# Kernel optimization log

Hardware: AMD Instinct MI355X
Metric: run time of the kernel (lower is better)

Reference implementation:

```python
import jax, jax.numpy as jnp
import numpy as np

B, A, D = 256, 128, 5          # batch, max_atoms, max_degree
FA, FB, C = 256, 64, 256       # atom feats, bond feats, conv_width


def setup_inputs() -> dict:
    key = jax.random.key(0)
    k1, k2, k3, k4 = jax.random.split(key, 4)
    atoms = jax.random.normal(k1, (B, A, FA), dtype=jnp.float32)
    bonds = jax.random.normal(k2, (B, A, D, FB), dtype=jnp.float32)
    # neighbour indices with -1 as padding value
    edges = jax.random.randint(k3, (B, A, D), -1, A, dtype=jnp.int32)
    W = jax.random.normal(k4, (D, FA + FB, C), dtype=jnp.float32) * 0.05
    b = jnp.zeros((D, C), dtype=jnp.float32)
    return {"atoms": atoms, "bonds": bonds, "edges": edges, "W": W, "b": b}


def reference(atoms, bonds, edges, W, b):
    # atom degree = number of non-padding neighbours  (B, A)
    deg = jnp.sum(edges != -1, axis=-1)

    # neighbour_lookup: pad a zero atom at index 0, shift indices by +1 so -1 -> 0
    masked_atoms = jnp.pad(atoms, ((0, 0), (1, 0), (0, 0)))        # (B, A+1, FA)
    idx = edges + 1                                                # (B, A, D)
    neigh = masked_atoms[jnp.arange(B)[:, None, None], idx]        # (B, A, D, FA)

    # include_self=True then sum over neighbour axis == self + sum(neighbours)
    summed_atom = atoms + jnp.sum(neigh, axis=2)                   # (B, A, FA)
    summed_bond = jnp.sum(bonds, axis=2)                           # (B, A, FB)
    feat = jnp.concatenate([summed_atom, summed_bond], axis=-1)    # (B, A, FA+FB)

    # per-degree Dense (relu), masked by (degree == d), summed over degrees
    dense = jax.nn.relu(jnp.einsum('baf,dfc->badc', feat, W) + b)  # (B, A, D, C)
    mask = (deg[..., None] == jnp.arange(D)).astype(dense.dtype)   # (B, A, D)
    return jnp.einsum('badc,bad->bac', dense, mask)                # (B, A, C)
```

## Files before the change

kernel.cpp:

```cpp
#include <hip/hip_runtime.h>


#define NB 256
#define NA 128
#define ND 5
#define NFA 256
#define NFB 64
#define NC 256
#define NF (NFA + NFB)

__global__ __launch_bounds__(256) void ngh_kernel(
    const float* __restrict__ atoms,
    const float* __restrict__ bonds,
    const int*   __restrict__ edges,
    const float* __restrict__ W,
    const float* __restrict__ bias,
    float* __restrict__ out)
{
    const int row = blockIdx.x;
    const int b   = row >> 7;
    const int a   = row & (NA - 1);
    const int t   = threadIdx.x;

    int e[ND];
    int deg = 0;
#pragma unroll
    for (int d = 0; d < ND; ++d) {
        e[d] = edges[row * ND + d];
        deg += (e[d] != -1) ? 1 : 0;
    }

    float* orow = out + (size_t)row * NC;

    if (deg >= ND) {
        orow[t] = 0.0f;
        return;
    }

    __shared__ float feat[NF];
    {
        const float* arow = atoms + ((size_t)b * NA + a) * NFA;
        float v = arow[t];
#pragma unroll
        for (int d = 0; d < ND; ++d) {
            if (e[d] != -1) {
                v += atoms[((size_t)b * NA + e[d]) * NFA + t];
            }
        }
        feat[t] = v;
    }
    if (t < NFB) {
        const float* brow = bonds + ((size_t)b * NA + a) * (ND * NFB);
        float v = 0.0f;
#pragma unroll
        for (int d = 0; d < ND; ++d) v += brow[d * NFB + t];
        feat[NFA + t] = v;
    }
    __syncthreads();

    const float* Wd = W + (size_t)deg * NF * NC + t;
    float acc = bias[deg * NC + t];
#pragma unroll 8
    for (int f = 0; f < NF; ++f) {
        acc = fmaf(feat[f], Wd[(size_t)f * NC], acc);
    }
    orow[t] = fmaxf(acc, 0.0f);
}

extern "C" void kernel_launch(void* const* d_in, const int* in_sizes, int n_in,
                              void* d_out, int out_size, void* d_ws, size_t ws_size,
                              hipStream_t stream) {
    const float* atoms = (const float*)d_in[0];
    const float* bonds = (const float*)d_in[1];
    const int*   edges = (const int*)  d_in[2];
    const float* W     = (const float*)d_in[3];
    const float* bias  = (const float*)d_in[4];
    float*       out   = (float*)d_out;

    dim3 grid(NB * NA);
    dim3 block(NC);
    ngh_kernel<<<grid, block, 0, stream>>>(atoms, bonds, edges, W, bias, out);
}
```

Baseline: 134.3 us.

## Bucket rows by degree and batch four rows per block for shared W reuse

A scan kernel zeroes the output and sorts row indices into per-degree lists with atomics. A persistent gather-matmul kernel then processes four same-degree rows per block, so each W element loaded is reused across four rows instead of one. This cuts W traffic roughly fourfold, at the cost of an extra memset, an extra launch and atomic list building. It falls back to the old kernel when no workspace is available.

New measurement: 147.9 us. 10.1% more time.

```diff
diff --git a/kernel.cpp b/kernel.cpp
--- a/kernel.cpp
+++ b/kernel.cpp
@@ -8,14 +8,14 @@
 #define NFB 64
 #define NC 256
 #define NF (NFA + NFB)
+#define NROWS (NB * NA)
+#define RPB 16
+#define RPC 4
 
 __global__ __launch_bounds__(256) void ngh_kernel(
-    const float* __restrict__ atoms,
-    const float* __restrict__ bonds,
-    const int*   __restrict__ edges,
-    const float* __restrict__ W,
-    const float* __restrict__ bias,
-    float* __restrict__ out)
+    const float* __restrict__ atoms, const float* __restrict__ bonds,
+    const int* __restrict__ edges, const float* __restrict__ W,
+    const float* __restrict__ bias, float* __restrict__ out)
 {
     const int row = blockIdx.x;
     const int b   = row >> 7;
@@ -31,22 +31,15 @@
     }
 
     float* orow = out + (size_t)row * NC;
-
-    if (deg >= ND) {
-        orow[t] = 0.0f;
-        return;
-    }
+    if (deg >= ND) { orow[t] = 0.0f; return; }
 
     __shared__ float feat[NF];
     {
         const float* arow = atoms + ((size_t)b * NA + a) * NFA;
         float v = arow[t];
 #pragma unroll
-        for (int d = 0; d < ND; ++d) {
-            if (e[d] != -1) {
-                v += atoms[((size_t)b * NA + e[d]) * NFA + t];
-            }
-        }
+        for (int d = 0; d < ND; ++d)
+            if (e[d] != -1) v += atoms[((size_t)b * NA + e[d]) * NFA + t];
         feat[t] = v;
     }
     if (t < NFB) {
@@ -61,10 +54,111 @@
     const float* Wd = W + (size_t)deg * NF * NC + t;
     float acc = bias[deg * NC + t];
 #pragma unroll 8
-    for (int f = 0; f < NF; ++f) {
-        acc = fmaf(feat[f], Wd[(size_t)f * NC], acc);
+    for (int f = 0; f < NF; ++f) acc = fmaf(feat[f], Wd[(size_t)f * NC], acc);
+    orow[t] = fmaxf(acc, 0.0f);
+}
+
+__global__ __launch_bounds__(256) void scan_zero_kernel(
+    const int* __restrict__ edges, float* __restrict__ out,
+    int* __restrict__ cnt, int* __restrict__ list)
+{
+    const int t  = threadIdx.x;
+    const int r0 = blockIdx.x * RPB;
+
+    float4* dst = reinterpret_cast<float4*>(out + (size_t)r0 * NC);
+    const float4 z = make_float4(0.f, 0.f, 0.f, 0.f);
+#pragma unroll
+    for (int k = 0; k < (RPB * NC / 4) / 256; ++k) dst[t + k * 256] = z;
+
+    if (t < RPB) {
+        const int row = r0 + t;
+        const int* er = edges + row * ND;
+        int deg = 0;
+#pragma unroll
+        for (int d = 0; d < ND; ++d) deg += (er[d] != -1) ? 1 : 0;
+        if (deg < ND) {
+            const int pos = atomicAdd(&cnt[deg], 1);
+            list[deg * NROWS + pos] = row;
+        }
     }
-    orow[t] = fmaxf(acc, 0.0f);
+}
+
+__global__ __launch_bounds__(256) void gather_mm_kernel(
+    const float* __restrict__ atoms, const float* __restrict__ bonds,
+    const int* __restrict__ edges, const float* __restrict__ W,
+    const float* __restrict__ bias, float* __restrict__ out,
+    const int* __restrict__ cnt, const int* __restrict__ list)
+{
+    __shared__ float feat[NF * RPC];
+    __shared__ int rows_s[RPC];
+    const int t = threadIdx.x;
+
+    int c[ND], base[ND], total = 0;
+#pragma unroll
+    for (int d = 0; d < ND; ++d) {
+        c[d]    = cnt[d];
+        base[d] = total;
+        total  += (c[d] + RPC - 1) / RPC;
+    }
+
+    for (int ci = blockIdx.x; ci < total; ci += gridDim.x) {
+        int deg = 0, j = 0;
+        bool found = false;
+#pragma unroll
+        for (int d = 0; d < ND; ++d) {
+            const int ch = (c[d] + RPC - 1) / RPC;
+            if (!found && ci < base[d] + ch) { deg = d; j = ci - base[d]; found = true; }
+        }
+        const int nrows = min(RPC, c[deg] - j * RPC);
+
+        if (t < RPC) rows_s[t] = (t < nrows) ? list[deg * NROWS + j * RPC + t] : -1;
+        __syncthreads();
+
+#pragma unroll
+        for (int r = 0; r < RPC; ++r) {
+            const int row = rows_s[r];
+            if (row >= 0) {
+                const int rb = row & ~(NA - 1);
+                const int* er = edges + row * ND;
+                float v = atoms[(size_t)row * NFA + t];
+#pragma unroll
+                for (int d = 0; d < ND; ++d) {
+                    const int e = er[d];
+                    if (e != -1) v += atoms[((size_t)(rb + e)) * NFA + t];
+                }
+                feat[t * RPC + r] = v;
+                if (t < NFB) {
+                    const float* br = bonds + (size_t)row * (ND * NFB) + t;
+                    feat[(NFA + t) * RPC + r] =
+                        br[0] + br[NFB] + br[2 * NFB] + br[3 * NFB] + br[4 * NFB];
+                }
+            }
+        }
+        __syncthreads();
+
+        float acc[RPC];
+        const float bv = bias[deg * NC + t];
+#pragma unroll
+        for (int r = 0; r < RPC; ++r) acc[r] = bv;
+
+        const float* Wd = W + (size_t)deg * (NF * NC) + t;
+#pragma unroll 8
+        for (int f = 0; f < NF; ++f) {
+            const float w = Wd[(size_t)f * NC];
+            const float4 fv = *reinterpret_cast<const float4*>(&feat[f * RPC]);
+            acc[0] = fmaf(fv.x, w, acc[0]);
+            acc[1] = fmaf(fv.y, w, acc[1]);
+            acc[2] = fmaf(fv.z, w, acc[2]);
+            acc[3] = fmaf(fv.w, w, acc[3]);
+        }
+
+#pragma unroll
+        for (int r = 0; r < RPC; ++r) {
+            const int row = rows_s[r];
+            if (row >= 0) out[(size_t)row * NC + t] = fmaxf(acc[r], 0.f);
+        }
+        __syncthreads();
+    }
 }
 
 extern "C" void kernel_launch(void* const* d_in, const int* in_sizes, int n_in,
@@ -77,7 +171,16 @@
     const float* bias  = (const float*)d_in[4];
     float*       out   = (float*)d_out;
 
-    dim3 grid(NB * NA);
-    dim3 block(NC);
-    ngh_kernel<<<grid, block, 0, stream>>>(atoms, bonds, edges, W, bias, out);
+    const size_t need = 64 + (size_t)ND * NROWS * sizeof(int);
+    if (d_ws == nullptr || ws_size < need) {
+        ngh_kernel<<<dim3(NROWS), dim3(NC), 0, stream>>>(atoms, bonds, edges, W, bias, out);
+        return;
+    }
+
+    int* cnt  = (int*)d_ws;
+    int* list = (int*)((char*)d_ws + 64);
+
+    hipMemsetAsync(cnt, 0, 64, stream);
+    scan_zero_kernel<<<dim3(NROWS / RPB), dim3(256), 0, stream>>>(edges, out, cnt, list);
+    gather_mm_kernel<<<dim3(1024), dim3(256), 0, stream>>>(atoms, bonds, edges, W, bias, out, cnt, list);
 }
```

## Bucket rows by degree per block and reuse weight loads across row chunks

Applied to the files above, without the earlier changes.

Each block now handles 64 rows. It zero-fills the output for those rows, then buckets the rows by degree in shared memory. For each degree it processes chunks of 8 rows, so each weight element loaded from global memory feeds 8 FMAs instead of one, cutting W traffic roughly eightfold. The cost is extra syncs, partial chunks when a degree bucket is small, and a redundant zero write followed by overwrites of the same output rows.

Result: slower. 150.9 us (+12.3%).

```diff
diff --git a/kernel.cpp b/kernel.cpp
--- a/kernel.cpp
+++ b/kernel.cpp
@@ -8,8 +8,12 @@
 #define NFB 64
 #define NC 256
 #define NF (NFA + NFB)
+#define NROWS (NB * NA)
+#define RPB 64
+#define RPC 8
+#define NBLK (NROWS / RPB)
 
-__global__ __launch_bounds__(256) void ngh_kernel(
+__global__ __launch_bounds__(256) void ngh_fused_kernel(
     const float* __restrict__ atoms,
     const float* __restrict__ bonds,
     const int*   __restrict__ edges,
@@ -17,54 +21,96 @@
     const float* __restrict__ bias,
     float* __restrict__ out)
 {
-    const int row = blockIdx.x;
-    const int b   = row >> 7;
-    const int a   = row & (NA - 1);
-    const int t   = threadIdx.x;
+    __shared__ float feat[NF * RPC];
+    __shared__ int   cnt_s[ND];
+    __shared__ int   lists[ND][RPB];
+    const int t  = threadIdx.x;
+    const int r0 = blockIdx.x * RPB;
 
-    int e[ND];
-    int deg = 0;
+    if (t < ND) cnt_s[t] = 0;
+
+    float4* dst = reinterpret_cast<float4*>(out + (size_t)r0 * NC);
+    const float4 z = make_float4(0.f, 0.f, 0.f, 0.f);
 #pragma unroll
-    for (int d = 0; d < ND; ++d) {
-        e[d] = edges[row * ND + d];
-        deg += (e[d] != -1) ? 1 : 0;
-    }
+    for (int k = 0; k < (RPB * NC / 4) / 256; ++k) dst[t + k * 256] = z;
 
-    float* orow = out + (size_t)row * NC;
+    __syncthreads();
 
-    if (deg >= ND) {
-        orow[t] = 0.0f;
-        return;
-    }
-
-    __shared__ float feat[NF];
-    {
-        const float* arow = atoms + ((size_t)b * NA + a) * NFA;
-        float v = arow[t];
+    if (t < RPB) {
+        const int row = r0 + t;
+        const int* er = edges + row * ND;
+        int deg = 0;
 #pragma unroll
-        for (int d = 0; d < ND; ++d) {
-            if (e[d] != -1) {
-                v += atoms[((size_t)b * NA + e[d]) * NFA + t];
-            }
+        for (int d = 0; d < ND; ++d) deg += (er[d] != -1) ? 1 : 0;
+        if (deg < ND) {
+            const int p = atomicAdd(&cnt_s[deg], 1);
+            lists[deg][p] = row;
         }
-        feat[t] = v;
-    }
-    if (t < NFB) {
-        const float* brow = bonds + ((size_t)b * NA + a) * (ND * NFB);
-        float v = 0.0f;
-#pragma unroll
-        for (int d = 0; d < ND; ++d) v += brow[d * NFB + t];
-        feat[NFA + t] = v;
     }
     __syncthreads();
 
-    const float* Wd = W + (size_t)deg * NF * NC + t;
-    float acc = bias[deg * NC + t];
-#pragma unroll 8
-    for (int f = 0; f < NF; ++f) {
-        acc = fmaf(feat[f], Wd[(size_t)f * NC], acc);
+    for (int d = 0; d < ND; ++d) {
+        const int n = cnt_s[d];
+        for (int j0 = 0; j0 < n; j0 += RPC) {
+            const int nr = min(RPC, n - j0);
+            int rows_r[RPC];
+#pragma unroll
+            for (int r = 0; r < RPC; ++r)
+                rows_r[r] = (r < nr) ? lists[d][j0 + r] : -1;
+
+#pragma unroll
+            for (int r = 0; r < RPC; ++r) {
+                const int row = rows_r[r];
+                float v = 0.f;
+                if (row >= 0) {
+                    const int rb = row & ~(NA - 1);
+                    const int* er = edges + row * ND;
+                    v = atoms[(size_t)row * NFA + t];
+#pragma unroll
+                    for (int dd = 0; dd < ND; ++dd) {
+                        const int e = er[dd];
+                        if (e != -1) v += atoms[(size_t)(rb + e) * NFA + t];
+                    }
+                }
+                feat[t * RPC + r] = v;
+                if (t < NFB) {
+                    float bs = 0.f;
+                    if (row >= 0) {
+                        const float* br = bonds + (size_t)row * (ND * NFB) + t;
+#pragma unroll
+                        for (int dd = 0; dd < ND; ++dd) bs += br[dd * NFB];
+                    }
+                    feat[(NFA + t) * RPC + r] = bs;
+                }
+            }
+            __syncthreads();
+
+            const float* Wd = W + (size_t)d * (NF * NC) + t;
+            const float bv = bias[d * NC + t];
+            float acc[RPC];
+#pragma unroll
+            for (int r = 0; r < RPC; ++r) acc[r] = bv;
+#pragma unroll 4
+            for (int f = 0; f < NF; ++f) {
+                const float w = Wd[(size_t)f * NC];
+                const float4 p0 = *reinterpret_cast<const float4*>(&feat[f * RPC]);
+                const float4 p1 = *reinterpret_cast<const float4*>(&feat[f * RPC + 4]);
+                acc[0] = fmaf(p0.x, w, acc[0]);
+                acc[1] = fmaf(p0.y, w, acc[1]);
+                acc[2] = fmaf(p0.z, w, acc[2]);
+                acc[3] = fmaf(p0.w, w, acc[3]);
+                acc[4] = fmaf(p1.x, w, acc[4]);
+                acc[5] = fmaf(p1.y, w, acc[5]);
+                acc[6] = fmaf(p1.z, w, acc[6]);
+                acc[7] = fmaf(p1.w, w, acc[7]);
+            }
+#pragma unroll
+            for (int r = 0; r < RPC; ++r)
+                if (rows_r[r] >= 0)
+                    out[(size_t)rows_r[r] * NC + t] = fmaxf(acc[r], 0.f);
+            __syncthreads();
+        }
     }
-    orow[t] = fmaxf(acc, 0.0f);
 }
 
 extern "C" void kernel_launch(void* const* d_in, const int* in_sizes, int n_in,
@@ -77,7 +123,6 @@
     const float* bias  = (const float*)d_in[4];
     float*       out   = (float*)d_out;
 
-    dim3 grid(NB * NA);
-    dim3 block(NC);
-    ngh_kernel<<<grid, block, 0, stream>>>(atoms, bonds, edges, W, bias, out);
+    ngh_fused_kernel<<<dim3(NBLK), dim3(256), 0, stream>>>(
+        atoms, bonds, edges, W, bias, out);
 }
```

## Process eight rows per block with split-K float4 GEMV and shared reduction

Applied to the files above, without the earlier changes.

Each block now handles eight atom rows instead of one. Within a row, the four waves split the feature dimension and each lane computes four output channels from float4 loads of W, and the partial sums are reduced through shared memory. This is meant to cut per-block launch overhead and widen W loads. In exchange, rows inside a block run one after another with several barriers each, which reduces block-level parallelism, and W is still reread from cache for every row.

Result: no change. 136.7 us (+1.8%).

```diff
diff --git a/kernel.cpp b/kernel.cpp
--- a/kernel.cpp
+++ b/kernel.cpp
@@ -8,6 +8,9 @@
 #define NFB 64
 #define NC 256
 #define NF (NFA + NFB)
+#define NROWS (NB * NA)
+#define RPB 8
+#define NBLK (NROWS / RPB)
 
 __global__ __launch_bounds__(256) void ngh_kernel(
     const float* __restrict__ atoms,
@@ -17,54 +20,107 @@
     const float* __restrict__ bias,
     float* __restrict__ out)
 {
-    const int row = blockIdx.x;
-    const int b   = row >> 7;
-    const int a   = row & (NA - 1);
-    const int t   = threadIdx.x;
+    __shared__ alignas(16) float  feat[NF];
+    __shared__ alignas(16) float4 red[4][NC / 4];
+    __shared__ int                eds[RPB * ND];
 
-    int e[ND];
-    int deg = 0;
+    const int t  = threadIdx.x;
+    const int r0 = blockIdx.x * RPB;
+    const int w  = t >> 6;
+    const int l  = t & 63;
+
+    if (t < RPB * ND) eds[t] = edges[r0 * ND + t];
+    __syncthreads();
+
+    unsigned needy = 0;
 #pragma unroll
-    for (int d = 0; d < ND; ++d) {
-        e[d] = edges[row * ND + d];
-        deg += (e[d] != -1) ? 1 : 0;
+    for (int r = 0; r < RPB; ++r) {
+        int dg = 0;
+#pragma unroll
+        for (int d = 0; d < ND; ++d) dg += (eds[r * ND + d] != -1) ? 1 : 0;
+        needy |= (dg < ND) ? (1u << r) : 0u;
     }
 
-    float* orow = out + (size_t)row * NC;
+#pragma unroll
+    for (int r = 0; r < RPB; ++r)
+        if (!((needy >> r) & 1u))
+            out[(size_t)(r0 + r) * NC + t] = 0.0f;
 
-    if (deg >= ND) {
-        orow[t] = 0.0f;
-        return;
-    }
+    if (needy == 0u) return;
 
-    __shared__ float feat[NF];
-    {
-        const float* arow = atoms + ((size_t)b * NA + a) * NFA;
-        float v = arow[t];
+    for (int r = 0; r < RPB; ++r) {
+        if (!((needy >> r) & 1u)) continue;
+        const int row = r0 + r;
+
+        int e[ND];
+        int deg = 0;
 #pragma unroll
         for (int d = 0; d < ND; ++d) {
-            if (e[d] != -1) {
-                v += atoms[((size_t)b * NA + e[d]) * NFA + t];
+            e[d] = eds[r * ND + d];
+            deg += (e[d] != -1) ? 1 : 0;
+        }
+
+        {
+            const int rb = row & ~(NA - 1);
+            float v = atoms[(size_t)row * NFA + t];
+#pragma unroll
+            for (int d = 0; d < ND; ++d)
+                if (e[d] != -1) v += atoms[(size_t)(rb + e[d]) * NFA + t];
+            feat[t] = v;
+            if (t < NFB) {
+                const float* br = bonds + (size_t)row * (ND * NFB) + t;
+                feat[NFA + t] = br[0] + br[NFB] + br[2 * NFB]
+                              + br[3 * NFB] + br[4 * NFB];
             }
         }
-        feat[t] = v;
+        __syncthreads();
+
+        const float* Wd = W + (size_t)deg * (NF * NC);
+        float4 acc = make_float4(0.f, 0.f, 0.f, 0.f);
+        const int fbase = w * (NF / 4);
+#pragma unroll 2
+        for (int fi = 0; fi < NF / 4; fi += 4) {
+            const int f = fbase + fi;
+            const float4 fv = *reinterpret_cast<const float4*>(&feat[f]);
+            const float4 w0 = *reinterpret_cast<const float4*>(&Wd[(size_t)(f + 0) * NC + l * 4]);
+            const float4 w1 = *reinterpret_cast<const float4*>(&Wd[(size_t)(f + 1) * NC + l * 4]);
+            const float4 w2 = *reinterpret_cast<const float4*>(&Wd[(size_t)(f + 2) * NC + l * 4]);
+            const float4 w3 = *reinterpret_cast<const float4*>(&Wd[(size_t)(f + 3) * NC + l * 4]);
+            acc.x = fmaf(fv.x, w0.x, acc.x);
+            acc.y = fmaf(fv.x, w0.y, acc.y);
+            acc.z = fmaf(fv.x, w0.z, acc.z);
+            acc.w = fmaf(fv.x, w0.w, acc.w);
+            acc.x = fmaf(fv.y, w1.x, acc.x);
+            acc.y = fmaf(fv.y, w1.y, acc.y);
+            acc.z = fmaf(fv.y, w1.z, acc.z);
+            acc.w = fmaf(fv.y, w1.w, acc.w);
+            acc.x = fmaf(fv.z, w2.x, acc.x);
+            acc.y = fmaf(fv.z, w2.y, acc.y);
+            acc.z = fmaf(fv.z, w2.z, acc.z);
+            acc.w = fmaf(fv.z, w2.w, acc.w);
+            acc.x = fmaf(fv.w, w3.x, acc.x);
+            acc.y = fmaf(fv.w, w3.y, acc.y);
+            acc.z = fmaf(fv.w, w3.z, acc.z);
+            acc.w = fmaf(fv.w, w3.w, acc.w);
+        }
+        red[w][l] = acc;
+        __syncthreads();
+
+        if (t < NC / 4) {
+            const float4 s0 = red[0][t];
+            const float4 s1 = red[1][t];
+            const float4 s2 = red[2][t];
+            const float4 s3 = red[3][t];
+            const float4 bv = *reinterpret_cast<const float4*>(&bias[deg * NC + t * 4]);
+            float4 o;
+            o.x = fmaxf(s0.x + s1.x + s2.x + s3.x + bv.x, 0.f);
+            o.y = fmaxf(s0.y + s1.y + s2.y + s3.y + bv.y, 0.f);
+            o.z = fmaxf(s0.z + s1.z + s2.z + s3.z + bv.z, 0.f);
+            o.w = fmaxf(s0.w + s1.w + s2.w + s3.w + bv.w, 0.f);
+            *reinterpret_cast<float4*>(&out[(size_t)row * NC + t * 4]) = o;
+        }
+        __syncthreads();
     }
-    if (t < NFB) {
-        const float* brow = bonds + ((size_t)b * NA + a) * (ND * NFB);
-        float v = 0.0f;
-#pragma unroll
-        for (int d = 0; d < ND; ++d) v += brow[d * NFB + t];
-        feat[NFA + t] = v;
-    }
-    __syncthreads();
-
-    const float* Wd = W + (size_t)deg * NF * NC + t;
-    float acc = bias[deg * NC + t];
-#pragma unroll 8
-    for (int f = 0; f < NF; ++f) {
-        acc = fmaf(feat[f], Wd[(size_t)f * NC], acc);
-    }
-    orow[t] = fmaxf(acc, 0.0f);
 }
 
 extern "C" void kernel_launch(void* const* d_in, const int* in_sizes, int n_in,
@@ -77,7 +133,6 @@
     const float* bias  = (const float*)d_in[4];
     float*       out   = (float*)d_out;
 
-    dim3 grid(NB * NA);
-    dim3 block(NC);
-    ngh_kernel<<<grid, block, 0, stream>>>(atoms, bonds, edges, W, bias, out);
+    ngh_kernel<<<dim3(NBLK), dim3(256), 0, stream>>>(
+        atoms, bonds, edges, W, bias, out);
 }
```
